# Kernel tuning notes

Hardware: AMD Instinct MI355X
Metric: run time of the kernel (lower is better)

Reference implementation:

```python
import jax, jax.numpy as jnp
import numpy as np

N, E, H, ED, GD = 100000, 1600000, 128, 64, 64
LN_EPS = 1e-5


def setup_inputs() -> dict:
    key = jax.random.key(0)
    ks = jax.random.split(key, 16)
    s = lambda d: 1.0 / np.sqrt(d)
    return {
        "node_state": jax.random.normal(ks[0], (N, H), jnp.float32),
        "edge_index": jax.random.randint(ks[1], (2, E), 0, N, jnp.int64),
        "edge_state": jax.random.normal(ks[2], (E, ED), jnp.float32),
        "global_state": jax.random.normal(ks[3], (GD,), jnp.float32),
        "msg_w1": jax.random.normal(ks[4], (H + ED + GD, H), jnp.float32) * s(H + ED + GD),
        "msg_b1": jnp.zeros((H,), jnp.float32),
        "msg_w2": jax.random.normal(ks[5], (H, H), jnp.float32) * s(H),
        "msg_b2": jnp.zeros((H,), jnp.float32),
        "upd_w1": jax.random.normal(ks[6], (2 * H + GD, H), jnp.float32) * s(2 * H + GD),
        "upd_b1": jnp.zeros((H,), jnp.float32),
        "upd_w2": jax.random.normal(ks[7], (H, H), jnp.float32) * s(H),
        "upd_b2": jnp.zeros((H,), jnp.float32),
        "ln_gamma": jnp.ones((H,), jnp.float32),
        "ln_beta": jnp.zeros((H,), jnp.float32),
    }


def _mlp(x, w1, b1, w2, b2):
    return jax.nn.relu(x @ w1 + b1) @ w2 + b2


def reference(node_state, edge_index, edge_state, global_state,
              msg_w1, msg_b1, msg_w2, msg_b2,
              upd_w1, upd_b1, upd_w2, upd_b2,
              ln_gamma, ln_beta):
    src, dst = edge_index[0], edge_index[1]
    num_nodes = node_state.shape[0]
    num_edges = src.shape[0]

    global_edges = jnp.broadcast_to(global_state, (num_edges, global_state.shape[0]))
    message_input = jnp.concatenate([node_state[src], edge_state, global_edges], axis=-1)
    messages = _mlp(message_input, msg_w1, msg_b1, msg_w2, msg_b2)  # [E, H]

    aggregated = jax.ops.segment_sum(messages, dst, num_segments=num_nodes)  # [N, H]
    degree = jax.ops.segment_sum(jnp.ones((num_edges,), node_state.dtype), dst,
                                 num_segments=num_nodes)  # [N]
    aggregated = aggregated / jnp.maximum(degree, 1.0)[:, None]

    global_nodes = jnp.broadcast_to(global_state, (num_nodes, global_state.shape[0]))
    update_input = jnp.concatenate([node_state, aggregated, global_nodes], axis=-1)
    delta = _mlp(update_input, upd_w1, upd_b1, upd_w2, upd_b2)

    x = node_state + delta
    mu = jnp.mean(x, axis=-1, keepdims=True)
    var = jnp.mean(jnp.square(x - mu), axis=-1, keepdims=True)
    return (x - mu) * jax.lax.rsqrt(var + LN_EPS) * ln_gamma + ln_beta
```

## Files before the change

kernel.cpp:

```cpp
#include <hip/hip_runtime.h>
#include <hip/hip_bf16.h>
#include <stdint.h>

#define NN 100000
#define NE 1600000

typedef __attribute__((ext_vector_type(4))) float f32x4;
typedef __attribute__((ext_vector_type(8))) __bf16 bf16x8;
typedef __attribute__((ext_vector_type(8))) short s16x8;
typedef __attribute__((ext_vector_type(4))) unsigned int u32x4;

__device__ __forceinline__ unsigned short f2bf(float f) {
  unsigned int u = __builtin_bit_cast(unsigned int, f);
  u += 0x7fffu + ((u >> 16) & 1u);
  return (unsigned short)(u >> 16);
}

__device__ __forceinline__ f32x4 mfma16(bf16x8 a, bf16x8 b, f32x4 c) {
  return __builtin_amdgcn_mfma_f32_16x16x32_bf16(a, b, c, 0, 0, 0);
}

__global__ void convert_kernel(const float* __restrict__ w1, const float* __restrict__ w2,
                               const float* __restrict__ g,
                               unsigned short* __restrict__ w1b, unsigned short* __restrict__ w2b,
                               unsigned short* __restrict__ gb)
{
  const int tid = blockIdx.x * 256 + threadIdx.x;
  if (tid < 256 * 128) w1b[tid] = f2bf(w1[tid]);
  if (tid < 128 * 128) w2b[tid] = f2bf(w2[tid]);
  if (tid < 64) gb[tid] = f2bf(g[tid]);
}

__global__ __launch_bounds__(256, 2) void edge_kernel(
    const int* __restrict__ ei,
    const float* __restrict__ edge_state,
    const float* __restrict__ node_state,
    const unsigned short* __restrict__ w1b,
    const unsigned short* __restrict__ w2b,
    const float* __restrict__ bias1g,
    const float* __restrict__ bias2g,
    const unsigned short* __restrict__ gb,
    float* __restrict__ agg,
    float* __restrict__ deg)
{
  __shared__ unsigned short sX[64 * 256];
  __shared__ unsigned short sH[64 * 128];
  __shared__ int sDst[64];

  const int t = threadIdx.x;
  const int lane = t & 63;
  const int wv = t >> 6;
  const int l15 = lane & 15;
  const int lq = lane >> 4;

  bf16x8 b1f[8][2], b2f[4][2];
  float bs1[2], bs2[2];
  for (int n = 0; n < 2; ++n) {
    const int col = wv * 32 + n * 16 + l15;
    bs1[n] = bias1g[col];
    bs2[n] = bias2g[col];
    for (int ks = 0; ks < 8; ++ks) {
      const int k0 = ks * 32 + lq * 8;
      s16x8 v;
#pragma unroll
      for (int j = 0; j < 8; ++j) v[j] = (short)w1b[(k0 + j) * 128 + col];
      b1f[ks][n] = __builtin_bit_cast(bf16x8, v);
    }
    for (int ks = 0; ks < 4; ++ks) {
      const int k0 = ks * 32 + lq * 8;
      s16x8 v;
#pragma unroll
      for (int j = 0; j < 8; ++j) v[j] = (short)w2b[(k0 + j) * 128 + col];
      b2f[ks][n] = __builtin_bit_cast(bf16x8, v);
    }
  }

  const int r = t >> 2;
  const int p = t & 3;
  const int rs = r & 7;

  for (int tile = blockIdx.x; tile < NE / 64; tile += gridDim.x) {
    __syncthreads();
    const int e0 = tile * 64;

    const int src = ei[e0 + r];
    if (p == 0) {
      const int d = ei[NE + e0 + r];
      sDst[r] = d;
      atomicAdd(&deg[d], 1.0f);
    }
    {
      const f32x4* nsv = (const f32x4*)(node_state + (size_t)src * 128 + p * 32);
#pragma unroll
      for (int j = 0; j < 4; ++j) {
        f32x4 x0 = nsv[2 * j], x1 = nsv[2 * j + 1];
        unsigned short buf[8];
#pragma unroll
        for (int i = 0; i < 4; ++i) { buf[i] = f2bf(x0[i]); buf[4 + i] = f2bf(x1[i]); }
        const int c = p * 4 + j;
        *(u32x4*)((char*)sX + r * 512 + ((c ^ rs) * 16)) = *(u32x4*)buf;
      }
    }
    {
      const f32x4* es = (const f32x4*)(edge_state + (size_t)e0 * 64 + r * 64 + p * 16);
      f32x4 e0v = es[0], e1v = es[1], e2v = es[2], e3v = es[3];
      unsigned short bufa[8], bufb[8];
#pragma unroll
      for (int i = 0; i < 4; ++i) {
        bufa[i] = f2bf(e0v[i]); bufa[4 + i] = f2bf(e1v[i]);
        bufb[i] = f2bf(e2v[i]); bufb[4 + i] = f2bf(e3v[i]);
      }
      const int c = 16 + 2 * p;
      *(u32x4*)((char*)sX + r * 512 + ((c ^ rs) * 16)) = *(u32x4*)bufa;
      *(u32x4*)((char*)sX + r * 512 + (((c + 1) ^ rs) * 16)) = *(u32x4*)bufb;
    }
    {
      const u32x4* g = (const u32x4*)(gb + p * 16);
      const int c = 24 + 2 * p;
      *(u32x4*)((char*)sX + r * 512 + ((c ^ rs) * 16)) = g[0];
      *(u32x4*)((char*)sX + r * 512 + (((c + 1) ^ rs) * 16)) = g[1];
    }
    __syncthreads();

    f32x4 acc[4][2];
#pragma unroll
    for (int m = 0; m < 4; ++m)
#pragma unroll
      for (int n = 0; n < 2; ++n)
        acc[m][n] = (f32x4){bs1[n], bs1[n], bs1[n], bs1[n]};
#pragma unroll
    for (int ks = 0; ks < 8; ++ks) {
      bf16x8 a[4];
#pragma unroll
      for (int m = 0; m < 4; ++m) {
        const int row = m * 16 + l15;
        a[m] = *(const bf16x8*)((const char*)sX + row * 512 + (((4 * ks + lq) ^ (row & 7)) * 16));
      }
#pragma unroll
      for (int m = 0; m < 4; ++m)
#pragma unroll
        for (int n = 0; n < 2; ++n)
          acc[m][n] = mfma16(a[m], b1f[ks][n], acc[m][n]);
    }
#pragma unroll
    for (int m = 0; m < 4; ++m)
#pragma unroll
      for (int n = 0; n < 2; ++n)
#pragma unroll
        for (int i = 0; i < 4; ++i) {
          const int row = m * 16 + lq * 4 + i;
          const int col = wv * 32 + n * 16 + l15;
          float v = acc[m][n][i];
          v = v > 0.f ? v : 0.f;
          *(unsigned short*)((char*)sH + row * 256 +
                             ((((col >> 3) ^ (row & 7)) * 16) + (col & 7) * 2)) = f2bf(v);
        }
    __syncthreads();

    f32x4 acc2[4][2];
#pragma unroll
    for (int m = 0; m < 4; ++m)
#pragma unroll
      for (int n = 0; n < 2; ++n)
        acc2[m][n] = (f32x4){bs2[n], bs2[n], bs2[n], bs2[n]};
#pragma unroll
    for (int ks = 0; ks < 4; ++ks) {
      bf16x8 a[4];
#pragma unroll
      for (int m = 0; m < 4; ++m) {
        const int row = m * 16 + l15;
        a[m] = *(const bf16x8*)((const char*)sH + row * 256 + (((4 * ks + lq) ^ (row & 7)) * 16));
      }
#pragma unroll
      for (int m = 0; m < 4; ++m)
#pragma unroll
        for (int n = 0; n < 2; ++n)
          acc2[m][n] = mfma16(a[m], b2f[ks][n], acc2[m][n]);
    }
#pragma unroll
    for (int m = 0; m < 4; ++m)
#pragma unroll
      for (int i = 0; i < 4; ++i) {
        const int row = m * 16 + lq * 4 + i;
        const int d = sDst[row];
#pragma unroll
        for (int n = 0; n < 2; ++n) {
          const int col = wv * 32 + n * 16 + l15;
          atomicAdd(&agg[(size_t)d * 128 + col], acc2[m][n][i]);
        }
      }
  }
}

__global__ __launch_bounds__(128, 3) void upd1_kernel(
    const float* __restrict__ node_state,
    const float* __restrict__ agg,
    const float* __restrict__ deg,
    const float* __restrict__ u1,
    const float* __restrict__ b1,
    const float* __restrict__ gs,
    float* __restrict__ h1out)
{
  const int n = blockIdx.x * 128 + threadIdx.x;
  const bool act = n < NN;
  const size_t row = (size_t)(act ? n : 0) * 128;

  f32x4 acc[32];
#pragma unroll
  for (int c = 0; c < 32; ++c) acc[c] = *(const f32x4*)(b1 + 4 * c);

  const float rdeg = act ? (1.0f / fmaxf(deg[n], 1.0f)) : 0.0f;

  for (int k4 = 0; k4 < 32; ++k4) {
    const f32x4 x = *(const f32x4*)(node_state + row + 4 * k4);
#pragma unroll
    for (int kk = 0; kk < 4; ++kk) {
      const float xk = x[kk];
      const float* wr = u1 + (size_t)(4 * k4 + kk) * 128;
#pragma unroll
      for (int c = 0; c < 32; ++c) acc[c] += xk * *(const f32x4*)(wr + 4 * c);
    }
  }
  for (int k4 = 0; k4 < 32; ++k4) {
    const f32x4 x = *(const f32x4*)(agg + row + 4 * k4);
#pragma unroll
    for (int kk = 0; kk < 4; ++kk) {
      const float xk = x[kk] * rdeg;
      const float* wr = u1 + (size_t)(128 + 4 * k4 + kk) * 128;
#pragma unroll
      for (int c = 0; c < 32; ++c) acc[c] += xk * *(const f32x4*)(wr + 4 * c);
    }
  }
  for (int k = 0; k < 64; ++k) {
    const float xk = gs[k];
    const float* wr = u1 + (size_t)(256 + k) * 128;
#pragma unroll
    for (int c = 0; c < 32; ++c) acc[c] += xk * *(const f32x4*)(wr + 4 * c);
  }

  if (act) {
    float* o = h1out + (size_t)n * 128;
#pragma unroll
    for (int c = 0; c < 32; ++c) {
      f32x4 v = acc[c];
#pragma unroll
      for (int i = 0; i < 4; ++i) v[i] = v[i] > 0.f ? v[i] : 0.f;
      *(f32x4*)(o + 4 * c) = v;
    }
  }
}

__global__ __launch_bounds__(128, 3) void upd2_kernel(
    const float* __restrict__ node_state,
    const float* __restrict__ h1,
    const float* __restrict__ u2,
    const float* __restrict__ b2,
    const float* __restrict__ lng,
    const float* __restrict__ lnb,
    float* __restrict__ out)
{
  const int n = blockIdx.x * 128 + threadIdx.x;
  const bool act = n < NN;
  const size_t row = (size_t)(act ? n : 0) * 128;

  f32x4 acc[32];
#pragma unroll
  for (int c = 0; c < 32; ++c) acc[c] = *(const f32x4*)(b2 + 4 * c);

  for (int k4 = 0; k4 < 32; ++k4) {
    const f32x4 h = *(const f32x4*)(h1 + row + 4 * k4);
#pragma unroll
    for (int kk = 0; kk < 4; ++kk) {
      const float hk = h[kk];
      const float* wr = u2 + (size_t)(4 * k4 + kk) * 128;
#pragma unroll
      for (int c = 0; c < 32; ++c) acc[c] += hk * *(const f32x4*)(wr + 4 * c);
    }
  }

  if (act) {
    float s = 0.f, s2 = 0.f;
#pragma unroll
    for (int c = 0; c < 32; ++c) {
      const f32x4 nd = *(const f32x4*)(node_state + row + 4 * c);
      f32x4 x = nd + acc[c];
      acc[c] = x;
#pragma unroll
      for (int i = 0; i < 4; ++i) { s += x[i]; s2 += x[i] * x[i]; }
    }
    const float mu = s * (1.0f / 128.0f);
    float var = s2 * (1.0f / 128.0f) - mu * mu;
    var = var < 0.f ? 0.f : var;
    const float rstd = rsqrtf(var + 1e-5f);
    float* o = out + (size_t)n * 128;
#pragma unroll
    for (int c = 0; c < 32; ++c) {
      const f32x4 g = *(const f32x4*)(lng + 4 * c);
      const f32x4 b = *(const f32x4*)(lnb + 4 * c);
      f32x4 x = acc[c];
#pragma unroll
      for (int i = 0; i < 4; ++i) x[i] = (x[i] - mu) * rstd * g[i] + b[i];
      *(f32x4*)(o + 4 * c) = x;
    }
  }
}

extern "C" void kernel_launch(void* const* d_in, const int* in_sizes, int n_in,
                              void* d_out, int out_size, void* d_ws, size_t ws_size,
                              hipStream_t stream)
{
  const float* node_state = (const float*)d_in[0];
  const int* ei           = (const int*)d_in[1];
  const float* edge_state = (const float*)d_in[2];
  const float* gstate     = (const float*)d_in[3];
  const float* msg_w1     = (const float*)d_in[4];
  const float* msg_b1     = (const float*)d_in[5];
  const float* msg_w2     = (const float*)d_in[6];
  const float* msg_b2     = (const float*)d_in[7];
  const float* upd_w1     = (const float*)d_in[8];
  const float* upd_b1     = (const float*)d_in[9];
  const float* upd_w2     = (const float*)d_in[10];
  const float* upd_b2     = (const float*)d_in[11];
  const float* ln_g       = (const float*)d_in[12];
  const float* ln_b       = (const float*)d_in[13];

  char* ws = (char*)d_ws;
  float* agg              = (float*)(ws + 0);
  float* deg              = (float*)(ws + 51200000);
  float* h1buf            = (float*)(ws + 51600000);
  unsigned short* w1b     = (unsigned short*)(ws + 102800000);
  unsigned short* w2b     = (unsigned short*)(ws + 102865536);
  unsigned short* gb      = (unsigned short*)(ws + 102898304);
  (void)ws_size; (void)in_sizes; (void)n_in; (void)out_size;

  hipMemsetAsync(ws, 0, 51600000, stream);
  hipLaunchKernelGGL(convert_kernel, dim3(128), dim3(256), 0, stream,
                     msg_w1, msg_w2, gstate, w1b, w2b, gb);
  hipLaunchKernelGGL(edge_kernel, dim3(512), dim3(256), 0, stream,
                     ei, edge_state, node_state, w1b, w2b, msg_b1, msg_b2, gb, agg, deg);
  hipLaunchKernelGGL(upd1_kernel, dim3((NN + 127) / 128), dim3(128), 0, stream,
                     node_state, agg, deg, upd_w1, upd_b1, gstate, h1buf);
  hipLaunchKernelGGL(upd2_kernel, dim3((NN + 127) / 128), dim3(128), 0, stream,
                     node_state, h1buf, upd_w2, upd_b2, ln_g, ln_b, (float*)d_out);
}
```

Measured before the change: 1.167 ms.

## Overlap node-only update GEMM partial with edge kernel via extra blocks

Splits the first update-MLP layer into a part that depends only on node_state and global_state and a part that depends on the aggregated messages. The node-only part now runs in extra blocks appended to the edge kernel's grid, so it can overlap with the edge message computation. A later kernel adds the aggregation contribution to that partial result. This adds a 51 MB intermediate buffer with an extra write and read, and the extra blocks compete with edge blocks for compute units and registers.

```diff
diff --git a/kernel.cpp b/kernel.cpp
--- a/kernel.cpp
+++ b/kernel.cpp
@@ -4,6 +4,8 @@
 
 #define NN 100000
 #define NE 1600000
+#define EDGE_GRID 512
+#define UPDA_BLOCKS 391
 
 typedef __attribute__((ext_vector_type(4))) float f32x4;
 typedef __attribute__((ext_vector_type(8))) __bf16 bf16x8;
@@ -31,7 +33,7 @@
   if (tid < 64) gb[tid] = f2bf(g[tid]);
 }
 
-__global__ __launch_bounds__(256, 2) void edge_kernel(
+__global__ __launch_bounds__(256, 2) void fused_kernel(
     const int* __restrict__ ei,
     const float* __restrict__ edge_state,
     const float* __restrict__ node_state,
@@ -41,13 +43,51 @@
     const float* __restrict__ bias2g,
     const unsigned short* __restrict__ gb,
     float* __restrict__ agg,
-    float* __restrict__ deg)
+    float* __restrict__ deg,
+    const float* __restrict__ u1,
+    const float* __restrict__ ub1,
+    const float* __restrict__ gs,
+    float* __restrict__ hpart)
 {
   __shared__ unsigned short sX[64 * 256];
   __shared__ unsigned short sH[64 * 128];
   __shared__ int sDst[64];
 
   const int t = threadIdx.x;
+
+  if (blockIdx.x >= EDGE_GRID) {
+    const int n = (blockIdx.x - EDGE_GRID) * 256 + t;
+    const bool act = n < NN;
+    const size_t row = (size_t)(act ? n : 0) * 128;
+
+    f32x4 acc[32];
+#pragma unroll
+    for (int c = 0; c < 32; ++c) acc[c] = *(const f32x4*)(ub1 + 4 * c);
+
+    for (int k4 = 0; k4 < 32; ++k4) {
+      const f32x4 x = *(const f32x4*)(node_state + row + 4 * k4);
+#pragma unroll
+      for (int kk = 0; kk < 4; ++kk) {
+        const float xk = x[kk];
+        const float* wr = u1 + (size_t)(4 * k4 + kk) * 128;
+#pragma unroll
+        for (int c = 0; c < 32; ++c) acc[c] += xk * *(const f32x4*)(wr + 4 * c);
+      }
+    }
+    for (int k = 0; k < 64; ++k) {
+      const float xk = gs[k];
+      const float* wr = u1 + (size_t)(256 + k) * 128;
+#pragma unroll
+      for (int c = 0; c < 32; ++c) acc[c] += xk * *(const f32x4*)(wr + 4 * c);
+    }
+    if (act) {
+      float* o = hpart + (size_t)n * 128;
+#pragma unroll
+      for (int c = 0; c < 32; ++c) *(f32x4*)(o + 4 * c) = acc[c];
+    }
+    return;
+  }
+
   const int lane = t & 63;
   const int wv = t >> 6;
   const int l15 = lane & 15;
@@ -79,7 +119,7 @@
   const int p = t & 3;
   const int rs = r & 7;
 
-  for (int tile = blockIdx.x; tile < NE / 64; tile += gridDim.x) {
+  for (int tile = blockIdx.x; tile < NE / 64; tile += EDGE_GRID) {
     __syncthreads();
     const int e0 = tile * 64;
 
@@ -192,13 +232,11 @@
   }
 }
 
-__global__ __launch_bounds__(128, 3) void upd1_kernel(
-    const float* __restrict__ node_state,
+__global__ __launch_bounds__(128, 3) void updB_kernel(
+    const float* __restrict__ hpart,
     const float* __restrict__ agg,
     const float* __restrict__ deg,
     const float* __restrict__ u1,
-    const float* __restrict__ b1,
-    const float* __restrict__ gs,
     float* __restrict__ h1out)
 {
   const int n = blockIdx.x * 128 + threadIdx.x;
@@ -207,20 +245,10 @@
 
   f32x4 acc[32];
 #pragma unroll
-  for (int c = 0; c < 32; ++c) acc[c] = *(const f32x4*)(b1 + 4 * c);
+  for (int c = 0; c < 32; ++c) acc[c] = *(const f32x4*)(hpart + row + 4 * c);
 
   const float rdeg = act ? (1.0f / fmaxf(deg[n], 1.0f)) : 0.0f;
 
-  for (int k4 = 0; k4 < 32; ++k4) {
-    const f32x4 x = *(const f32x4*)(node_state + row + 4 * k4);
-#pragma unroll
-    for (int kk = 0; kk < 4; ++kk) {
-      const float xk = x[kk];
-      const float* wr = u1 + (size_t)(4 * k4 + kk) * 128;
-#pragma unroll
-      for (int c = 0; c < 32; ++c) acc[c] += xk * *(const f32x4*)(wr + 4 * c);
-    }
-  }
   for (int k4 = 0; k4 < 32; ++k4) {
     const f32x4 x = *(const f32x4*)(agg + row + 4 * k4);
 #pragma unroll
@@ -230,12 +258,6 @@
 #pragma unroll
       for (int c = 0; c < 32; ++c) acc[c] += xk * *(const f32x4*)(wr + 4 * c);
     }
-  }
-  for (int k = 0; k < 64; ++k) {
-    const float xk = gs[k];
-    const float* wr = u1 + (size_t)(256 + k) * 128;
-#pragma unroll
-    for (int c = 0; c < 32; ++c) acc[c] += xk * *(const f32x4*)(wr + 4 * c);
   }
 
   if (act) {
@@ -327,19 +349,21 @@
   char* ws = (char*)d_ws;
   float* agg              = (float*)(ws + 0);
   float* deg              = (float*)(ws + 51200000);
-  float* h1buf            = (float*)(ws + 51600000);
-  unsigned short* w1b     = (unsigned short*)(ws + 102800000);
-  unsigned short* w2b     = (unsigned short*)(ws + 102865536);
-  unsigned short* gb      = (unsigned short*)(ws + 102898304);
+  float* hpart            = (float*)(ws + 51600000);
+  float* h1buf            = (float*)(ws + 102800000);
+  unsigned short* w1b     = (unsigned short*)(ws + 154000000);
+  unsigned short* w2b     = (unsigned short*)(ws + 154065536);
+  unsigned short* gb      = (unsigned short*)(ws + 154098304);
   (void)ws_size; (void)in_sizes; (void)n_in; (void)out_size;
 
   hipMemsetAsync(ws, 0, 51600000, stream);
-  hipLaunchKernelGGL(convert_kernel, dim3(128), dim3(256), 0, stream,
+  hipLaunchKernelGGL(convert_kernel, dim3(160), dim3(256), 0, stream,
                      msg_w1, msg_w2, gstate, w1b, w2b, gb);
-  hipLaunchKernelGGL(edge_kernel, dim3(512), dim3(256), 0, stream,
-                     ei, edge_state, node_state, w1b, w2b, msg_b1, msg_b2, gb, agg, deg);
-  hipLaunchKernelGGL(upd1_kernel, dim3((NN + 127) / 128), dim3(128), 0, stream,
-                     node_state, agg, deg, upd_w1, upd_b1, gstate, h1buf);
+  hipLaunchKernelGGL(fused_kernel, dim3(EDGE_GRID + UPDA_BLOCKS), dim3(256), 0, stream,
+                     ei, edge_state, node_state, w1b, w2b, msg_b1, msg_b2, gb,
+                     agg, deg, upd_w1, upd_b1, gstate, hpart);
+  hipLaunchKernelGGL(updB_kernel, dim3((NN + 127) / 128), dim3(128), 0, stream,
+                     hpart, agg, deg, upd_w1, h1buf);
   hipLaunchKernelGGL(upd2_kernel, dim3((NN + 127) / 128), dim3(128), 0, stream,
                      node_state, h1buf, upd_w2, upd_b2, ln_g, ln_b, (float*)d_out);
 }
```

New measurement: 1.128 ms. 3.4% less time.
